# Optimization experiments

Hardware: AMD Instinct MI355X
Metric: run time of the kernel (lower is better)

Reference implementation:

```python
import jax, jax.numpy as jnp
import numpy as np

DT = 1e-3   # timestep (s)
DH = 10.0   # grid spacing (m)


def setup_inputs() -> dict:
    key = jax.random.key(0)
    k1, k2, k3, k4 = jax.random.split(key, 4)
    B, NT, NZ, NX, NREC = 8, 256, 256, 256, 64
    x = jax.random.normal(k1, (B, NT), dtype=jnp.float32)            # source wavelets
    vp = 1500.0 + 2000.0 * jax.random.uniform(k2, (NZ, NX), dtype=jnp.float32)
    src_loc = jax.random.randint(k3, (B, 2), 4, NZ - 4, dtype=jnp.int32)        # (z,x) per shot
    rec_loc = jax.random.randint(k4, (B, NREC, 2), 4, NZ - 4, dtype=jnp.int32)  # (z,x) per rec
    return {"x": x, "vp": vp, "src_loc": src_loc, "rec_loc": rec_loc}


def reference(x, vp, src_loc, rec_loc):
    """Acoustic 2nd-order leapfrog FD time-stepping (WaveRNN pattern):
    per step: stencil update -> source scatter-inject -> receiver gather.
    Returns receiver traces (B, NT, NREC)."""
    B, NT = x.shape
    nz, nx = vp.shape
    c2dt2 = (vp * vp) * jnp.float32(DT * DT)   # (nz, nx), broadcast over batch
    inv_dh2 = jnp.float32(1.0 / (DH * DH))
    bidx = jnp.arange(B)
    sz, sx = src_loc[:, 0], src_loc[:, 1]
    rz, rx = rec_loc[..., 0], rec_loc[..., 1]

    def laplacian(h):  # 5-point stencil, zero (Dirichlet) boundaries
        interior = (h[:, 2:, 1:-1] + h[:, :-2, 1:-1]
                    + h[:, 1:-1, 2:] + h[:, 1:-1, :-2]
                    - 4.0 * h[:, 1:-1, 1:-1]) * inv_dh2
        return jnp.zeros_like(h).at[:, 1:-1, 1:-1].set(interior)

    def step(carry, wav_t):
        h1, h2 = carry                              # fields at t, t-1
        hn = 2.0 * h1 - h2 + c2dt2 * laplacian(h1)  # leapfrog update
        hn = hn.at[bidx, sz, sx].add(jnp.float32(DT * DT) * wav_t)  # source inject
        rec = hn[bidx[:, None], rz, rx]             # receiver gather (B, NREC)
        return (hn, h1), rec

    h0 = jnp.zeros((B, nz, nx), dtype=x.dtype)
    _, recs = jax.lax.scan(step, (h0, h0), x.T)     # recs: (NT, B, NREC)
    return jnp.transpose(recs, (1, 0, 2))           # (B, NT, NREC)
```

## Files before the change

### kernel.cpp

```cpp
#include <hip/hip_runtime.h>

typedef float v4f __attribute__((ext_vector_type(4)));

namespace {
constexpr int B_     = 8;
constexpr int NT_    = 256;
constexpr int NX_    = 256;
constexpr int NREC_  = 64;
constexpr int PIECES = 32;
constexpr int IROWS  = 8;
constexpr int G      = 16;
constexpr int ROUNDS = NT_ / G;
constexpr int NBANDS = 5;
constexpr int NTHR   = NBANDS * 64;
constexpr int NBLK   = B_ * PIECES;
constexpr float DT2  = 1e-6f;
constexpr float KLAP = 1e-8f;
constexpr size_t FLAGS_BYTES = 4096;
constexpr int RCAP = 6;
}

__device__ __forceinline__ float dpp_shr1(float v) {
    return __int_as_float(__builtin_amdgcn_update_dpp(
        0, __float_as_int(v), 0x138 , 0xF, 0xF, true));
}
__device__ __forceinline__ float dpp_shl1(float v) {
    return __int_as_float(__builtin_amdgcn_update_dpp(
        0, __float_as_int(v), 0x130 , 0xF, 0xF, true));
}

__device__ __forceinline__ void store_v4_sys(float* p, v4f v) {
    asm volatile("global_store_dwordx4 %0, %1, off sc0 sc1"
                 :: "v"(p), "v"(v) : "memory");
}
__device__ __forceinline__ v4f load_v4_sys(const float* p) {
    v4f r;
    asm volatile("global_load_dwordx4 %0, %1, off sc0 sc1"
                 : "=v"(r) : "v"(p) : "memory");
    return r;
}

extern "C" __global__
__attribute__((amdgpu_flat_work_group_size(NTHR, NTHR), amdgpu_waves_per_eu(2, 4)))
void wave_reg_kernel(const float* __restrict__ x,
                     const float* __restrict__ vp,
                     const int* __restrict__ src_loc,
                     const int* __restrict__ rec_loc,
                     float* __restrict__ out,
                     int* __restrict__ flags,
                     float* __restrict__ gbuf)
{
    __shared__ float pub[2][2][NBANDS][256];
    __shared__ float wav[NT_];
    __shared__ float recbuf[G][NREC_];
    __shared__ unsigned char recown[NREC_];

    const int bid  = blockIdx.x;
    const int b    = bid & 7;
    const int p    = bid >> 3;
    const int blk  = b * PIECES + p;
    const int tid  = threadIdx.x;
    const int band = tid >> 6;
    const int lane = tid & 63;
    const int c0   = lane << 2;
    const int grt  = p * IROWS - G + (band << 3);

    const int cut = (band < 2) ? ((band << 3) + 7)
                  : ((band == 2) ? 16 : (((4 - band) << 3) + 7));

    if (tid < NT_) wav[tid] = x[b * NT_ + tid];
    if (tid < NREC_) {
        int rz = rec_loc[(b * NREC_ + tid) * 2 + 0];
        recown[tid] = (rz >= p * IROWS && rz < p * IROWS + IROWS) ? 1 : 0;
    }

    v4f cf[8], cf2[8];
#pragma unroll
    for (int i = 0; i < 8; ++i) {
        int gr = grt + i;
        int crow = gr < 0 ? 0 : (gr > 255 ? 255 : gr);
        bool rowok = (gr >= 1) && (gr <= 254);
        v4f vv = *(const v4f*)&vp[crow * NX_ + c0];
        float cc[4];
#pragma unroll
        for (int k = 0; k < 4; ++k) {
            int col = c0 + k;
            float vk = (k == 0) ? vv.x : (k == 1) ? vv.y : (k == 2) ? vv.z : vv.w;
            cc[k] = (rowok && col >= 1 && col <= 254) ? vk * vk * KLAP : 0.f;
        }
        cf[i].x = cc[0]; cf[i].y = cc[1]; cf[i].z = cc[2]; cf[i].w = cc[3];
        cf2[i].x = 2.f - 4.f * cc[0]; cf2[i].y = 2.f - 4.f * cc[1];
        cf2[i].z = 2.f - 4.f * cc[2]; cf2[i].w = 2.f - 4.f * cc[3];
    }

    const int sz = src_loc[b * 2 + 0], sx = src_loc[b * 2 + 1];
    const int si = sz - grt;
    const int sj = sx - c0;
    const bool has_src = ((unsigned)si < 8u) && ((unsigned)sj < 4u);
    const bool wave_has_src = __any(has_src);

    int rs[RCAP]; int rcnt = 0;
#pragma unroll 1
    for (int r = 0; r < NREC_; ++r) {
        int rz = rec_loc[(b * NREC_ + r) * 2 + 0];
        int rx = rec_loc[(b * NREC_ + r) * 2 + 1];
        int i = rz - grt, j = rx - c0;
        if (rz >= p * IROWS && rz < p * IROWS + IROWS &&
            (unsigned)i < 8u && (unsigned)j < 4u) {
            if (rcnt < RCAP) rs[rcnt] = (r << 5) | (i << 2) | j;
            ++rcnt;
        }
    }
    if (rcnt > RCAP) rcnt = RCAP;
    const bool wave_has_rec = __any(rcnt > 0);
    float* outb = out + (size_t)b * NT_ * NREC_;

    v4f A[8], Bv[8];
    {
        v4f z = {0.f, 0.f, 0.f, 0.f};
#pragma unroll
        for (int i = 0; i < 8; ++i) { A[i] = z; Bv[i] = z; }
    }

    auto gptr = [&](int e, int bk, int lvl, int rr) -> float* {
        return gbuf + ((((size_t)(e & 1) * NBLK + bk) * 2 + lvl) * 8 + rr) * 256;
    };

#define ROW(I, NV, SV) do {                                                   \
    float wv = dpp_shr1(C[I].w);       \
    float ev = dpp_shl1(C[I].x);      \
    v4f hn;                                                                   \
    { float sm = ((NV).x + (SV).x) + (wv     + C[I].y);                       \
      hn.x = fmaf(cf[I].x, sm, fmaf(cf2[I].x, C[I].x, -P[I].x)); }            \
    { float sm = ((NV).y + (SV).y) + (C[I].x + C[I].z);                       \
      hn.y = fmaf(cf[I].y, sm, fmaf(cf2[I].y, C[I].y, -P[I].y)); }            \
    { float sm = ((NV).z + (SV).z) + (C[I].y + C[I].w);                       \
      hn.z = fmaf(cf[I].z, sm, fmaf(cf2[I].z, C[I].z, -P[I].z)); }            \
    { float sm = ((NV).w + (SV).w) + (C[I].z + ev);                           \
      hn.w = fmaf(cf[I].w, sm, fmaf(cf2[I].w, C[I].w, -P[I].w)); }            \
    P[I] = hn;                                                                \
} while (0)

    auto step = [&](v4f (&C)[8], v4f (&P)[8], int t, int par) {
        const int k = (t & (G - 1)) + 1;
        if (k <= cut + 1) {
            *(v4f*)&pub[par][0][band][c0] = C[0];
            *(v4f*)&pub[par][1][band][c0] = C[7];
        }
        __syncthreads();
        if (k > cut) return;
        v4f nn, ss;
        if (band > 0)          nn = *(const v4f*)&pub[par][1][band - 1][c0];
        else                   { nn.x = 0.f; nn.y = 0.f; nn.z = 0.f; nn.w = 0.f; }
        if (band < NBANDS - 1) ss = *(const v4f*)&pub[par][0][band + 1][c0];
        else                   { ss.x = 0.f; ss.y = 0.f; ss.z = 0.f; ss.w = 0.f; }
        ROW(1, C[0], C[2]);
        ROW(2, C[1], C[3]);
        ROW(3, C[2], C[4]);
        ROW(4, C[3], C[5]);
        ROW(5, C[4], C[6]);
        ROW(6, C[5], C[7]);
        ROW(0, nn,   C[1]);
        ROW(7, C[6], ss);
        if (wave_has_src) {
            const float sv = DT2 * wav[t];
#pragma unroll
            for (int i = 0; i < 8; ++i) {
                if (has_src && si == i) {
                    if      (sj == 0) P[i].x += sv;
                    else if (sj == 1) P[i].y += sv;
                    else if (sj == 2) P[i].z += sv;
                    else              P[i].w += sv;
                }
            }
        }
        if (wave_has_rec) {
#pragma unroll
            for (int kk = 0; kk < RCAP; ++kk) {
                if (rcnt > kk) {
                    int pk = rs[kk];
                    int i = (pk >> 2) & 7, j = pk & 3, r = pk >> 5;
                    v4f lo = (i & 2) ? ((i & 1) ? P[3] : P[2])
                                     : ((i & 1) ? P[1] : P[0]);
                    v4f hi = (i & 2) ? ((i & 1) ? P[7] : P[6])
                                     : ((i & 1) ? P[5] : P[4]);
                    v4f rw = (i & 4) ? hi : lo;
                    float c01 = (j & 1) ? rw.y : rw.x;
                    float c23 = (j & 1) ? rw.w : rw.z;
                    recbuf[t & (G - 1)][r] = (j & 2) ? c23 : c01;
                }
            }
        }
    };

    auto publish_prev = [&](int e) {
        if (band == 2) {
#pragma unroll
            for (int i = 0; i < 8; ++i)
                store_v4_sys(&gptr(e, blk, 1, i)[c0], Bv[i]);
        }
    };

    auto exchange = [&](int e) {
        if (band == 2) {
#pragma unroll
            for (int i = 0; i < 8; ++i)
                store_v4_sys(&gptr(e, blk, 0, i)[c0], A[i]);
        }
        __syncthreads();
        if (tid == 0)
            __hip_atomic_store(&flags[blk], e + 1, __ATOMIC_RELAXED,
                               __HIP_MEMORY_SCOPE_SYSTEM);
        if (band == 0 && p >= 2) {
            if (lane == 0)
                while (__hip_atomic_load(&flags[blk - 2], __ATOMIC_RELAXED,
                                         __HIP_MEMORY_SCOPE_SYSTEM) < e + 1)
                    __builtin_amdgcn_s_sleep(1);
#pragma unroll
            for (int i = 0; i < 8; ++i) {
                A[i]  = load_v4_sys(&gptr(e, blk - 2, 0, i)[c0]);
                Bv[i] = load_v4_sys(&gptr(e, blk - 2, 1, i)[c0]);
            }
        }
        if (band == 1 && p >= 1) {
            if (lane == 0)
                while (__hip_atomic_load(&flags[blk - 1], __ATOMIC_RELAXED,
                                         __HIP_MEMORY_SCOPE_SYSTEM) < e + 1)
                    __builtin_amdgcn_s_sleep(1);
#pragma unroll
            for (int i = 0; i < 8; ++i) {
                A[i]  = load_v4_sys(&gptr(e, blk - 1, 0, i)[c0]);
                Bv[i] = load_v4_sys(&gptr(e, blk - 1, 1, i)[c0]);
            }
        }
        if (band == 3 && p < PIECES - 1) {
            if (lane == 0)
                while (__hip_atomic_load(&flags[blk + 1], __ATOMIC_RELAXED,
                                         __HIP_MEMORY_SCOPE_SYSTEM) < e + 1)
                    __builtin_amdgcn_s_sleep(1);
#pragma unroll
            for (int i = 0; i < 8; ++i) {
                A[i]  = load_v4_sys(&gptr(e, blk + 1, 0, i)[c0]);
                Bv[i] = load_v4_sys(&gptr(e, blk + 1, 1, i)[c0]);
            }
        }
        if (band == 4 && p < PIECES - 2) {
            if (lane == 0)
                while (__hip_atomic_load(&flags[blk + 2], __ATOMIC_RELAXED,
                                         __HIP_MEMORY_SCOPE_SYSTEM) < e + 1)
                    __builtin_amdgcn_s_sleep(1);
#pragma unroll
            for (int i = 0; i < 8; ++i) {
                A[i]  = load_v4_sys(&gptr(e, blk + 2, 0, i)[c0]);
                Bv[i] = load_v4_sys(&gptr(e, blk + 2, 1, i)[c0]);
            }
        }
        asm volatile("s_waitcnt vmcnt(0)" ::: "memory");
        __builtin_amdgcn_sched_barrier(0);
        __syncthreads();
    };

    int t = 0;
#pragma unroll 1
    for (int e = 0; e < ROUNDS; ++e) {
#pragma unroll 1
        for (int s = 0; s < G; s += 2) {
            step(A, Bv, t, 0);
            if (s == G - 2 && e < ROUNDS - 1)
                publish_prev(e);
            step(Bv, A, t + 1, 1);
            t += 2;
        }
        __syncthreads();
#pragma unroll 1
        for (int idx = tid; idx < G * NREC_; idx += NTHR) {
            int s = idx >> 6, r = idx & 63;
            if (recown[r]) outb[(e * G + s) * NREC_ + r] = recbuf[s][r];
        }
        if (e < ROUNDS - 1) exchange(e);
    }
#undef ROW
}

extern "C" void kernel_launch(void* const* d_in, const int* in_sizes, int n_in,
                              void* d_out, int out_size, void* d_ws, size_t ws_size,
                              hipStream_t stream) {
    const float* x   = (const float*)d_in[0];
    const float* vp  = (const float*)d_in[1];
    const int*   src = (const int*)d_in[2];
    const int*   rec = (const int*)d_in[3];
    float*       o   = (float*)d_out;
    int*   flags = (int*)d_ws;
    float* gbuf  = (float*)((char*)d_ws + FLAGS_BYTES);
    (void)hipMemsetAsync(d_ws, 0, FLAGS_BYTES, stream);
    hipLaunchKernelGGL(wave_reg_kernel, dim3(NBLK), dim3(NTHR), 0, stream,
                       x, vp, src, rec, o, flags, gbuf);
}
```

Measured before the change: 310.4 us.

## Double piece height and halo depth to halve inter-block exchange rounds

Result: slower. 330.7 us (+6.5%).

```diff
diff --git a/kernel.cpp b/kernel.cpp
--- a/kernel.cpp
+++ b/kernel.cpp
@@ -7,11 +7,11 @@
 constexpr int NT_    = 256;
 constexpr int NX_    = 256;
 constexpr int NREC_  = 64;
-constexpr int PIECES = 32;
-constexpr int IROWS  = 8;
-constexpr int G      = 16;
+constexpr int PIECES = 16;
+constexpr int IROWS  = 16;
+constexpr int G      = 32;
 constexpr int ROUNDS = NT_ / G;
-constexpr int NBANDS = 5;
+constexpr int NBANDS = 10;
 constexpr int NTHR   = NBANDS * 64;
 constexpr int NBLK   = B_ * PIECES;
 constexpr float DT2  = 1e-6f;
@@ -65,8 +65,8 @@
     const int c0   = lane << 2;
     const int grt  = p * IROWS - G + (band << 3);
 
-    const int cut = (band < 2) ? ((band << 3) + 7)
-                  : ((band == 2) ? 16 : (((4 - band) << 3) + 7));
+    const int cut = (band < 4) ? ((band << 3) + 7)
+                  : ((band < 6) ? G : (79 - (band << 3)));
 
     if (tid < NT_) wav[tid] = x[b * NT_ + tid];
     if (tid < NREC_) {
@@ -123,7 +123,7 @@
     }
 
     auto gptr = [&](int e, int bk, int lvl, int rr) -> float* {
-        return gbuf + ((((size_t)(e & 1) * NBLK + bk) * 2 + lvl) * 8 + rr) * 256;
+        return gbuf + ((((size_t)(e & 1) * NBLK + bk) * 2 + lvl) * 16 + rr) * 256;
     };
 
 #define ROW(I, NV, SV) do {                                                   \
@@ -194,65 +194,71 @@
     };
 
     auto publish_prev = [&](int e) {
-        if (band == 2) {
+        if (band == 4 || band == 5) {
+            int rr0 = (band - 4) << 3;
 #pragma unroll
             for (int i = 0; i < 8; ++i)
-                store_v4_sys(&gptr(e, blk, 1, i)[c0], Bv[i]);
+                store_v4_sys(&gptr(e, blk, 1, rr0 + i)[c0], Bv[i]);
         }
     };
 
     auto exchange = [&](int e) {
-        if (band == 2) {
+        if (band == 4 || band == 5) {
+            int rr0 = (band - 4) << 3;
 #pragma unroll
             for (int i = 0; i < 8; ++i)
-                store_v4_sys(&gptr(e, blk, 0, i)[c0], A[i]);
+                store_v4_sys(&gptr(e, blk, 0, rr0 + i)[c0], A[i]);
         }
         __syncthreads();
         if (tid == 0)
             __hip_atomic_store(&flags[blk], e + 1, __ATOMIC_RELAXED,
                                __HIP_MEMORY_SCOPE_SYSTEM);
-        if (band == 0 && p >= 2) {
+        if (band < 2 && p >= 2) {
             if (lane == 0)
                 while (__hip_atomic_load(&flags[blk - 2], __ATOMIC_RELAXED,
                                          __HIP_MEMORY_SCOPE_SYSTEM) < e + 1)
                     __builtin_amdgcn_s_sleep(1);
-#pragma unroll
-            for (int i = 0; i < 8; ++i) {
-                A[i]  = load_v4_sys(&gptr(e, blk - 2, 0, i)[c0]);
-                Bv[i] = load_v4_sys(&gptr(e, blk - 2, 1, i)[c0]);
-            }
-        }
-        if (band == 1 && p >= 1) {
+            int rr0 = (band & 1) << 3;
+#pragma unroll
+            for (int i = 0; i < 8; ++i) {
+                A[i]  = load_v4_sys(&gptr(e, blk - 2, 0, rr0 + i)[c0]);
+                Bv[i] = load_v4_sys(&gptr(e, blk - 2, 1, rr0 + i)[c0]);
+            }
+        }
+        if (band >= 2 && band < 4 && p >= 1) {
             if (lane == 0)
                 while (__hip_atomic_load(&flags[blk - 1], __ATOMIC_RELAXED,
                                          __HIP_MEMORY_SCOPE_SYSTEM) < e + 1)
                     __builtin_amdgcn_s_sleep(1);
-#pragma unroll
-            for (int i = 0; i < 8; ++i) {
-                A[i]  = load_v4_sys(&gptr(e, blk - 1, 0, i)[c0]);
-                Bv[i] = load_v4_sys(&gptr(e, blk - 1, 1, i)[c0]);
-            }
-        }
-        if (band == 3 && p < PIECES - 1) {
+            int rr0 = (band & 1) << 3;
+#pragma unroll
+            for (int i = 0; i < 8; ++i) {
+                A[i]  = load_v4_sys(&gptr(e, blk - 1, 0, rr0 + i)[c0]);
+                Bv[i] = load_v4_sys(&gptr(e, blk - 1, 1, rr0 + i)[c0]);
+            }
+        }
+        if (band >= 6 && band < 8 && p < PIECES - 1) {
             if (lane == 0)
                 while (__hip_atomic_load(&flags[blk + 1], __ATOMIC_RELAXED,
                                          __HIP_MEMORY_SCOPE_SYSTEM) < e + 1)
                     __builtin_amdgcn_s_sleep(1);
-#pragma unroll
-            for (int i = 0; i < 8; ++i) {
-                A[i]  = load_v4_sys(&gptr(e, blk + 1, 0, i)[c0]);
-                Bv[i] = load_v4_sys(&gptr(e, blk + 1, 1, i)[c0]);
-            }
-        }
-        if (band == 4 && p < PIECES - 2) {
+            int rr0 = (band & 1) << 3;
+#pragma unroll
+            for (int i = 0; i < 8; ++i) {
+                A[i]  = load_v4_sys(&gptr(e, blk + 1, 0, rr0 + i)[c0]);
+                Bv[i] = load_v4_sys(&gptr(e, blk + 1, 1, rr0 + i)[c0]);
+            }
+        }
+        if (band >= 8 && p < PIECES - 2) {
             if (lane == 0)
                 while (__hip_atomic_load(&flags[blk + 2], __ATOMIC_RELAXED,
                                          __HIP_MEMORY_SCOPE_SYSTEM) < e + 1)
                     __builtin_amdgcn_s_sleep(1);
-#pragma unroll
-            for (int i = 0; i < 8; ++i) {
-                A[i]  = load_v4_sys(&gptr(e, blk + 2, 0, i)[c0]);
-                Bv[i] = load_v4_sys(&gptr(e, blk + 2, 1, i)[c0]);
+            int rr0 = (band & 1) << 3;
+#pragma unroll
+            for (int i = 0; i < 8; ++i) {
+                A[i]  = load_v4_sys(&gptr(e, blk + 2, 0, rr0 + i)[c0]);
+                Bv[i] = load_v4_sys(&gptr(e, blk + 2, 1, rr0 + i)[c0]);
             }
         }
         asm volatile("s_waitcnt vmcnt(0)" ::: "memory");
```
